# Performance work log

Hardware: AMD Instinct MI355X
Metric: run time of the kernel (lower is better)

The kernel has to match this reference:

```python
import jax, jax.numpy as jnp
import numpy as np


def conv1x1(x, w, b):
    # x: [B,C,H,W], w: [O,C], b: [O] -> [B,O,H,W]
    return jnp.einsum('bchw,oc->bohw', x, w) + b[None, :, None, None]


def setup_inputs() -> dict:
    key = jax.random.key(0)
    ks = jax.random.split(key, 8)
    B, C, H, W = 16, 256, 64, 64
    Cq = C // 8
    x = jax.random.normal(ks[0], (B, C, H, W), dtype=jnp.float32)
    wq = jax.random.normal(ks[1], (Cq, C), dtype=jnp.float32) * (2.0 / C) ** 0.5
    bq = jnp.zeros((Cq,), dtype=jnp.float32)
    wk = jax.random.normal(ks[2], (Cq, C), dtype=jnp.float32) * (2.0 / C) ** 0.5
    bk = jnp.zeros((Cq,), dtype=jnp.float32)
    wv = jax.random.normal(ks[3], (C, C), dtype=jnp.float32) * (2.0 / C) ** 0.5
    bv = jnp.zeros((C,), dtype=jnp.float32)
    gamma = jax.random.normal(ks[4], (1,), dtype=jnp.float32) * 0.1
    return {'x': x, 'wq': wq, 'bq': bq, 'wk': wk, 'bk': bk, 'wv': wv, 'bv': bv, 'gamma': gamma}


def reference(x, wq, bq, wk, bk, wv, bv, gamma):
    B, C, H, W = x.shape
    bH = B // 4
    bW = B // 4  # requires bH*bW == B, i.e. B == 16
    q = conv1x1(x, wq, bq)   # [B, C/8, H, W]
    k = conv1x1(x, wk, bk)   # [B, C/8, H, W]
    v = conv1x1(x, wv, bv)   # [B, C, H, W]
    # batch index b -> grid (h = b // bW, w = b % bW); token feature = flat map
    qg = q.reshape(bH, bW, -1)  # [bH, bW, Dq]
    kg = k.reshape(bH, bW, -1)
    vg = v.reshape(bH, bW, -1)  # [bH, bW, Dv]
    # column ('H') attention with -inf diagonal, row ('W') attention
    eH = jnp.einsum('hwd,gwd->hwg', qg, kg)  # [bH, bW, bH]
    eye = jnp.eye(bH, dtype=bool)[:, None, :]  # mask h == h'
    eH = jnp.where(eye, -jnp.inf, eH)
    eW = jnp.einsum('hwd,hgd->hwg', qg, kg)  # [bH, bW, bW]
    att = jax.nn.softmax(jnp.concatenate([eH, eW], axis=-1), axis=-1)
    aH, aW = att[..., :bH], att[..., bH:]
    oH = jnp.einsum('hwg,gwd->hwd', aH, vg)  # attend down the column
    oW = jnp.einsum('hwg,hgd->hwd', aW, vg)  # attend along the row
    out = (oH + oW).reshape(B, C, H, W)
    return gamma[0] * out + x
```

## Files before the change

kernel.cpp:

```cpp
#include <hip/hip_runtime.h>

#define HW_  4096
#define DV   1048576

using bf16x8 = __attribute__((ext_vector_type(8))) __bf16;
using f32x4  = __attribute__((ext_vector_type(4))) float;

static __device__ __forceinline__ unsigned short f2bf(float f) {
    union { float f; unsigned u; } v; v.f = f;
    unsigned r = v.u + 0x7FFFu + ((v.u >> 16) & 1u);
    return (unsigned short)(r >> 16);
}
static __device__ __forceinline__ float bf2f(unsigned short h) {
    union { unsigned u; float f; } v; v.u = ((unsigned)h) << 16;
    return v.f;
}

__global__ __launch_bounds__(256) void k_pack(const float* wq, const float* wk, const float* wv,
                                              unsigned short* WhF, unsigned short* WlF, unsigned short* WvF) {
    int idx = blockIdx.x * 256 + threadIdx.x;
    if (idx < 16384) {
        int i = idx;
        int mt = i >> 12, cg = (i >> 7) & 31, ml = (i >> 3) & 15, cl = i & 7;
        int m = mt * 16 + ml, c = cg * 8 + cl;
        float f = (m < 32) ? wq[m * 256 + c] : wk[(m - 32) * 256 + c];
        unsigned short hi = f2bf(f);
        WhF[i] = hi;
        WlF[i] = f2bf(f - bf2f(hi));
    } else {
        int i = idx - 16384;
        int mt = i >> 12, kt = (i >> 7) & 31, lr = (i >> 3) & 15, j = i & 7;
        int m = mt * 16 + lr, c = kt * 8 + j;
        WvF[i] = f2bf(wv[m * 256 + c]);
    }
}

__global__ __launch_bounds__(1024, 4) void k_qks(const unsigned short* __restrict__ WhF,
                                                 const unsigned short* __restrict__ WlF,
                                                 const float* __restrict__ x,
                                                 const float* __restrict__ bq, const float* __restrict__ bk,
                                                 float* __restrict__ Sp) {
    __shared__ __align__(16) __bf16 SB[2][16][2][1024];
    int n0 = blockIdx.x * 16;
    int t = threadIdx.x;
    int lane = t & 63, wid = t >> 6;
    int lr = lane & 15, kg = lane >> 4;
    int sn = t & 15, sk = t >> 4;
    int saddr = ((sk >> 3) * 16 + sn) * 8 + (sk & 7);

    f32x4 acc[4];
    #pragma unroll
    for (int mf = 0; mf < 4; mf++) acc[mf] = (f32x4){0.f, 0.f, 0.f, 0.f};

    float xv[16];
    const float* xs0 = x + (size_t)sk * HW_ + n0 + sn;
    #pragma unroll
    for (int bp = 0; bp < 16; bp++) xv[bp] = xs0[(size_t)bp * DV];
    #pragma unroll
    for (int bp = 0; bp < 16; bp++) {
        float v = xv[bp]; __bf16 h = (__bf16)v;
        SB[0][bp][0][saddr] = h;
        SB[0][bp][1][saddr] = (__bf16)(v - (float)h);
    }
    __syncthreads();

    const unsigned short* Abh = WhF + lane * 8;
    const unsigned short* Abl = WlF + lane * 8;

    for (int c = 0; c < 4; c++) {
        int cur = c & 1;
        if (c < 3) {
            const float* xp = x + (size_t)((c + 1) * 64 + sk) * HW_ + n0 + sn;
            #pragma unroll
            for (int bp = 0; bp < 16; bp++) xv[bp] = xp[(size_t)bp * DV];
        }
        #pragma unroll
        for (int sub = 0; sub < 2; sub++) {
            int kcg = c * 2 + sub;
            bf16x8 bh = *(const bf16x8*)&SB[cur][wid][0][sub * 512 + lane * 8];
            bf16x8 bl = *(const bf16x8*)&SB[cur][wid][1][sub * 512 + lane * 8];
            #pragma unroll
            for (int mf = 0; mf < 4; mf++) {
                bf16x8 ah = *(const bf16x8*)(Abh + mf * 4096 + kcg * 512);
                bf16x8 al = *(const bf16x8*)(Abl + mf * 4096 + kcg * 512);
                acc[mf] = __builtin_amdgcn_mfma_f32_16x16x32_bf16(ah, bh, acc[mf], 0, 0, 0);
                acc[mf] = __builtin_amdgcn_mfma_f32_16x16x32_bf16(ah, bl, acc[mf], 0, 0, 0);
                acc[mf] = __builtin_amdgcn_mfma_f32_16x16x32_bf16(al, bh, acc[mf], 0, 0, 0);
            }
        }
        if (c < 3) {
            int nb = cur ^ 1;
            #pragma unroll
            for (int bp = 0; bp < 16; bp++) {
                float v = xv[bp]; __bf16 h = (__bf16)v;
                SB[nb][bp][0][saddr] = h;
                SB[nb][bp][1][saddr] = (__bf16)(v - (float)h);
            }
        }
        __syncthreads();
    }

    __bf16* F = &SB[0][0][0][0];
    int b = wid;
    #pragma unroll
    for (int mf = 0; mf < 4; mf++) {
        #pragma unroll
        for (int i = 0; i < 4; i++) {
            int row64 = mf * 16 + kg * 4 + i;
            float val = acc[mf][i] + ((row64 < 32) ? bq[row64] : bk[row64 - 32]);
            int qk = row64 >> 5;
            int r  = row64 & 31;
            int col = r * 16 + lr;
            __bf16 h = (__bf16)val;
            __bf16 l = (__bf16)(val - (float)h);
            int base = qk * 16384 + ((col >> 3) * 16 + b) * 8 + (col & 7);
            F[base] = h;
            F[base + 8192] = l;
        }
    }
    __syncthreads();

    if (wid == 0) {
        f32x4 S = (f32x4){0.f, 0.f, 0.f, 0.f};
        #pragma unroll
        for (int s = 0; s < 16; s++) {
            bf16x8 qh = *(const bf16x8*)&F[s * 512 + lane * 8];
            bf16x8 ql = *(const bf16x8*)&F[8192 + s * 512 + lane * 8];
            bf16x8 kh = *(const bf16x8*)&F[16384 + s * 512 + lane * 8];
            bf16x8 kl = *(const bf16x8*)&F[24576 + s * 512 + lane * 8];
            S = __builtin_amdgcn_mfma_f32_16x16x32_bf16(qh, kh, S, 0, 0, 0);
            S = __builtin_amdgcn_mfma_f32_16x16x32_bf16(qh, kl, S, 0, 0, 0);
            S = __builtin_amdgcn_mfma_f32_16x16x32_bf16(ql, kh, S, 0, 0, 0);
        }
        #pragma unroll
        for (int i = 0; i < 4; i++) {
            int bb = kg * 4 + i;
            int bp = lr;
            int h = bb >> 2, w = bb & 3;
            float val = S[i];
            if ((bp & 3) == w) Sp[(size_t)blockIdx.x * 128 + bb * 8 + (bp >> 2)] = val;
            if ((bp >> 2) == h) Sp[(size_t)blockIdx.x * 128 + bb * 8 + 4 + (bp & 3)] = val;
        }
    }
}

__global__ void k_softmax3(const float* __restrict__ Sp, const float* __restrict__ gamma,
                           float* __restrict__ Mm) {
    __shared__ float SS[128];
    int t = threadIdx.x;
    float s = 0.f;
    #pragma unroll 8
    for (int blk = 0; blk < 256; blk++) s += Sp[(size_t)blk * 128 + t];
    SS[t] = s;
    __syncthreads();
    if (t < 16) {
        int b = t, h = b >> 2, w = b & 3;
        float e[8];
        for (int j = 0; j < 8; j++) e[j] = SS[b * 8 + j];
        e[h] = -INFINITY;
        float mx = e[0];
        for (int j = 1; j < 8; j++) mx = fmaxf(mx, e[j]);
        float aa[8], sum = 0.f;
        for (int j = 0; j < 8; j++) { aa[j] = expf(e[j] - mx); sum += aa[j]; }
        float inv = 1.0f / sum;
        float g = gamma[0];
        float row[16];
        for (int c = 0; c < 16; c++) row[c] = 0.f;
        for (int gg = 0; gg < 4; gg++) if (gg != h) row[gg * 4 + w] += aa[gg] * inv;
        for (int gg = 0; gg < 4; gg++) row[h * 4 + gg] += aa[4 + gg] * inv;
        for (int c = 0; c < 16; c++) Mm[b * 16 + c] = row[c] * g;
        Mm[256 + b] = g;
    }
}

__global__ __launch_bounds__(1024, 4) void k_fused(const unsigned short* __restrict__ WvF,
                                                   const float* __restrict__ x,
                                                   const float* __restrict__ bv,
                                                   const float* __restrict__ Mm,
                                                   float* __restrict__ out) {
    __shared__ __align__(16) __bf16 XB[2][16][1024];
    int n0 = blockIdx.x * 16;
    int t = threadIdx.x;
    int lane = t & 63, wid = t >> 6;
    int lr = lane & 15, kg = lane >> 4;
    int sn = t & 15, sk = t >> 4;
    int saddr = ((sk >> 3) * 16 + sn) * 8 + (sk & 7);

    f32x4 u[16];
    #pragma unroll
    for (int b = 0; b < 16; b++) u[b] = (f32x4){0.f, 0.f, 0.f, 0.f};

    float xv[16];
    const float* xs0 = x + (size_t)sk * HW_ + n0 + sn;
    #pragma unroll
    for (int bp = 0; bp < 16; bp++) xv[bp] = xs0[(size_t)bp * DV];
    #pragma unroll
    for (int bp = 0; bp < 16; bp++) XB[0][bp][saddr] = (__bf16)xv[bp];
    __syncthreads();

    const unsigned short* Ab = WvF + (size_t)wid * 4096 + lane * 8;

    for (int c = 0; c < 4; c++) {
        int cur = c & 1;
        if (c < 3) {
            const float* xp = x + (size_t)((c + 1) * 64 + sk) * HW_ + n0 + sn;
            #pragma unroll
            for (int bp = 0; bp < 16; bp++) xv[bp] = xp[(size_t)bp * DV];
        }
        #pragma unroll
        for (int sub = 0; sub < 2; sub++) {
            bf16x8 a = *(const bf16x8*)(Ab + (c * 2 + sub) * 512);
            #pragma unroll
            for (int b = 0; b < 16; b++) {
                bf16x8 bb = *(const bf16x8*)&XB[cur][b][sub * 512 + lane * 8];
                u[b] = __builtin_amdgcn_mfma_f32_16x16x32_bf16(a, bb, u[b], 0, 0, 0);
            }
        }
        if (c < 3) {
            int nb = cur ^ 1;
            #pragma unroll
            for (int bp = 0; bp < 16; bp++) XB[nb][bp][saddr] = (__bf16)xv[bp];
        }
        __syncthreads();
    }

    #pragma unroll
    for (int b = 0; b < 16; b++) {
        int h = b >> 2, w = b & 3;
        f32x4 m = (f32x4){0.f, 0.f, 0.f, 0.f};
        #pragma unroll
        for (int g = 0; g < 4; g++) {
            if (g != h) m += Mm[b * 16 + g * 4 + w] * u[g * 4 + w];
            m += Mm[b * 16 + h * 4 + g] * u[h * 4 + g];
        }
        float rs = Mm[256 + b];
        #pragma unroll
        for (int i = 0; i < 4; i++) {
            int mrow = wid * 16 + kg * 4 + i;
            size_t idx = (size_t)b * DV + (size_t)mrow * HW_ + n0 + lr;
            out[idx] = m[i] + rs * bv[mrow] + x[idx];
        }
    }
}

extern "C" void kernel_launch(void* const* d_in, const int* in_sizes, int n_in,
                              void* d_out, int out_size, void* d_ws, size_t ws_size,
                              hipStream_t stream) {
    (void)in_sizes; (void)n_in; (void)out_size; (void)ws_size;
    const float* x     = (const float*)d_in[0];
    const float* wq    = (const float*)d_in[1];
    const float* bq    = (const float*)d_in[2];
    const float* wk    = (const float*)d_in[3];
    const float* bk    = (const float*)d_in[4];
    const float* wv    = (const float*)d_in[5];
    const float* bv    = (const float*)d_in[6];
    const float* gamma = (const float*)d_in[7];

    char* ws = (char*)d_ws;
    unsigned short* WhF = (unsigned short*)(ws + 0);
    unsigned short* WlF = (unsigned short*)(ws + 32768);
    unsigned short* WvF = (unsigned short*)(ws + 65536);
    float*          Sp  = (float*)(ws + 196608);
    float*          Mm  = (float*)(ws + 327680);
    float*          vo  = (float*)d_out;

    k_pack     <<<320, 256, 0, stream>>>(wq, wk, wv, WhF, WlF, WvF);
    k_qks      <<<256, 1024, 0, stream>>>(WhF, WlF, x, bq, bk, Sp);
    k_softmax3 <<<1, 128, 0, stream>>>(Sp, gamma, Mm);
    k_fused    <<<256, 1024, 0, stream>>>(WvF, x, bv, Mm, vo);
}
```

Before: 103.2 us.

## Retile fused value kernel to 64x64 output tiles with vectorized loads and LDS-staged stores

The fused V-projection kernel now gives each block a 64-channel by 64-pixel tile across all 16 batches, instead of all 256 channels by 16 pixels. It iterates over 8 k-chunks with a swizzled LDS layout and float4 global loads of x. Output is staged through LDS so the residual add and final store run as coalesced float4 accesses. The Q/K score kernel also switches to float4 loads with a permuted LDS layout, and the partial-score buffer is transposed so the softmax reduction reads contiguous float4. The cost is a 128KB LDS footprint per block, which may reduce occupancy, plus extra LDS round trips in the epilogue.

```diff
diff --git a/kernel.cpp b/kernel.cpp
--- a/kernel.cpp
+++ b/kernel.cpp
@@ -40,27 +40,34 @@
                                                  const float* __restrict__ x,
                                                  const float* __restrict__ bq, const float* __restrict__ bk,
                                                  float* __restrict__ Sp) {
-    __shared__ __align__(16) __bf16 SB[2][16][2][1024];
+    __shared__ __align__(16) __bf16 SBf[2 * 16 * 2 * 1024];
     int n0 = blockIdx.x * 16;
     int t = threadIdx.x;
     int lane = t & 63, wid = t >> 6;
     int lr = lane & 15, kg = lane >> 4;
-    int sn = t & 15, sk = t >> 4;
-    int saddr = ((sk >> 3) * 16 + sn) * 8 + (sk & 7);
+    int n4 = t & 3, sk = (t >> 2) & 63, bpg = t >> 8;
+    int siglr = ((lr & 3) << 2) | (lr >> 2);
 
     f32x4 acc[4];
     #pragma unroll
     for (int mf = 0; mf < 4; mf++) acc[mf] = (f32x4){0.f, 0.f, 0.f, 0.f};
 
-    float xv[16];
-    const float* xs0 = x + (size_t)sk * HW_ + n0 + sn;
-    #pragma unroll
-    for (int bp = 0; bp < 16; bp++) xv[bp] = xs0[(size_t)bp * DV];
-    #pragma unroll
-    for (int bp = 0; bp < 16; bp++) {
-        float v = xv[bp]; __bf16 h = (__bf16)v;
-        SB[0][bp][0][saddr] = h;
-        SB[0][bp][1][saddr] = (__bf16)(v - (float)h);
+    f32x4 xv[4];
+    #pragma unroll
+    for (int bpi = 0; bpi < 4; bpi++)
+        xv[bpi] = *(const f32x4*)(x + (size_t)(bpg * 4 + bpi) * DV + (size_t)sk * HW_ + n0 + n4 * 4);
+    #pragma unroll
+    for (int bpi = 0; bpi < 4; bpi++) {
+        int bp = bpg * 4 + bpi;
+        __bf16* basep = SBf + ((0 * 16 + bp) * 2) * 1024 + (sk >> 5) * 512 + (((sk & 31) >> 3) * 16) * 8 + (sk & 7);
+        #pragma unroll
+        for (int e = 0; e < 4; e++) {
+            float v = xv[bpi][e];
+            __bf16 h = (__bf16)v;
+            int off = ((e << 2) | n4) * 8;
+            basep[off] = h;
+            basep[off + 1024] = (__bf16)(v - (float)h);
+        }
     }
     __syncthreads();
 
@@ -70,15 +77,16 @@
     for (int c = 0; c < 4; c++) {
         int cur = c & 1;
         if (c < 3) {
-            const float* xp = x + (size_t)((c + 1) * 64 + sk) * HW_ + n0 + sn;
-            #pragma unroll
-            for (int bp = 0; bp < 16; bp++) xv[bp] = xp[(size_t)bp * DV];
+            #pragma unroll
+            for (int bpi = 0; bpi < 4; bpi++)
+                xv[bpi] = *(const f32x4*)(x + (size_t)(bpg * 4 + bpi) * DV + (size_t)((c + 1) * 64 + sk) * HW_ + n0 + n4 * 4);
         }
         #pragma unroll
         for (int sub = 0; sub < 2; sub++) {
             int kcg = c * 2 + sub;
-            bf16x8 bh = *(const bf16x8*)&SB[cur][wid][0][sub * 512 + lane * 8];
-            bf16x8 bl = *(const bf16x8*)&SB[cur][wid][1][sub * 512 + lane * 8];
+            const __bf16* bptr = SBf + ((cur * 16 + wid) * 2) * 1024 + sub * 512 + (kg * 16 + siglr) * 8;
+            bf16x8 bh = *(const bf16x8*)bptr;
+            bf16x8 bl = *(const bf16x8*)(bptr + 1024);
             #pragma unroll
             for (int mf = 0; mf < 4; mf++) {
                 bf16x8 ah = *(const bf16x8*)(Abh + mf * 4096 + kcg * 512);
@@ -91,16 +99,23 @@
         if (c < 3) {
             int nb = cur ^ 1;
             #pragma unroll
-            for (int bp = 0; bp < 16; bp++) {
-                float v = xv[bp]; __bf16 h = (__bf16)v;
-                SB[nb][bp][0][saddr] = h;
-                SB[nb][bp][1][saddr] = (__bf16)(v - (float)h);
+            for (int bpi = 0; bpi < 4; bpi++) {
+                int bp = bpg * 4 + bpi;
+                __bf16* basep = SBf + ((nb * 16 + bp) * 2) * 1024 + (sk >> 5) * 512 + (((sk & 31) >> 3) * 16) * 8 + (sk & 7);
+                #pragma unroll
+                for (int e = 0; e < 4; e++) {
+                    float v = xv[bpi][e];
+                    __bf16 h = (__bf16)v;
+                    int off = ((e << 2) | n4) * 8;
+                    basep[off] = h;
+                    basep[off + 1024] = (__bf16)(v - (float)h);
+                }
             }
         }
         __syncthreads();
     }
 
-    __bf16* F = &SB[0][0][0][0];
+    __bf16* F = SBf;
     int b = wid;
     #pragma unroll
     for (int mf = 0; mf < 4; mf++) {
@@ -138,8 +153,8 @@
             int bp = lr;
             int h = bb >> 2, w = bb & 3;
             float val = S[i];
-            if ((bp & 3) == w) Sp[(size_t)blockIdx.x * 128 + bb * 8 + (bp >> 2)] = val;
-            if ((bp >> 2) == h) Sp[(size_t)blockIdx.x * 128 + bb * 8 + 4 + (bp & 3)] = val;
+            if ((bp & 3) == w)  Sp[(size_t)(bb * 8 + (bp >> 2)) * 256 + blockIdx.x] = val;
+            if ((bp >> 2) == h) Sp[(size_t)(bb * 8 + 4 + (bp & 3)) * 256 + blockIdx.x] = val;
         }
     }
 }
@@ -148,10 +163,11 @@
                            float* __restrict__ Mm) {
     __shared__ float SS[128];
     int t = threadIdx.x;
-    float s = 0.f;
+    const f32x4* s4 = (const f32x4*)(Sp + (size_t)t * 256);
+    f32x4 a = (f32x4){0.f, 0.f, 0.f, 0.f};
     #pragma unroll 8
-    for (int blk = 0; blk < 256; blk++) s += Sp[(size_t)blk * 128 + t];
-    SS[t] = s;
+    for (int i = 0; i < 64; i++) a += s4[i];
+    SS[t] = a[0] + a[1] + a[2] + a[3];
     __syncthreads();
     if (t < 16) {
         int b = t, h = b >> 2, w = b & 3;
@@ -178,68 +194,101 @@
                                                    const float* __restrict__ bv,
                                                    const float* __restrict__ Mm,
                                                    float* __restrict__ out) {
-    __shared__ __align__(16) __bf16 XB[2][16][1024];
-    int n0 = blockIdx.x * 16;
+    __shared__ __align__(16) char RAW[131072];
+    __bf16* XBf = (__bf16*)RAW;
+    int bid = blockIdx.x;
+    int xg = bid & 7, r = bid >> 3;
+    int nblk = xg * 8 + (r >> 2), mblk = r & 3;
+    int n0 = nblk * 64, m0 = mblk * 64;
     int t = threadIdx.x;
     int lane = t & 63, wid = t >> 6;
+    int wm = wid & 3, wn = wid >> 2;
     int lr = lane & 15, kg = lane >> 4;
-    int sn = t & 15, sk = t >> 4;
-    int saddr = ((sk >> 3) * 16 + sn) * 8 + (sk & 7);
+    int n4 = t & 15, sk = (t >> 4) & 31, bpg = t >> 9;
+    int sigr = (((lr & 3) << 2) | (lr >> 2)) ^ (wn << 1);
 
     f32x4 u[16];
     #pragma unroll
     for (int b = 0; b < 16; b++) u[b] = (f32x4){0.f, 0.f, 0.f, 0.f};
 
-    float xv[16];
-    const float* xs0 = x + (size_t)sk * HW_ + n0 + sn;
-    #pragma unroll
-    for (int bp = 0; bp < 16; bp++) xv[bp] = xs0[(size_t)bp * DV];
-    #pragma unroll
-    for (int bp = 0; bp < 16; bp++) XB[0][bp][saddr] = (__bf16)xv[bp];
+    f32x4 xv[8];
+    #pragma unroll
+    for (int bpi = 0; bpi < 8; bpi++)
+        xv[bpi] = *(const f32x4*)(x + (size_t)(bpg * 8 + bpi) * DV + (size_t)sk * HW_ + n0 + n4 * 4);
+    #pragma unroll
+    for (int bpi = 0; bpi < 8; bpi++) {
+        int bp = bpg * 8 + bpi;
+        __bf16* basep = XBf + ((0 * 16 + bp) * 4 + (n4 >> 2)) * 512 + ((sk >> 3) * 16) * 8 + (sk & 7);
+        #pragma unroll
+        for (int e = 0; e < 4; e++) {
+            int s = ((e << 2) | (n4 & 3)) ^ ((n4 >> 2) << 1);
+            basep[s * 8] = (__bf16)xv[bpi][e];
+        }
+    }
     __syncthreads();
 
-    const unsigned short* Ab = WvF + (size_t)wid * 4096 + lane * 8;
-
-    for (int c = 0; c < 4; c++) {
+    for (int c = 0; c < 8; c++) {
         int cur = c & 1;
-        if (c < 3) {
-            const float* xp = x + (size_t)((c + 1) * 64 + sk) * HW_ + n0 + sn;
-            #pragma unroll
-            for (int bp = 0; bp < 16; bp++) xv[bp] = xp[(size_t)bp * DV];
-        }
-        #pragma unroll
-        for (int sub = 0; sub < 2; sub++) {
-            bf16x8 a = *(const bf16x8*)(Ab + (c * 2 + sub) * 512);
-            #pragma unroll
-            for (int b = 0; b < 16; b++) {
-                bf16x8 bb = *(const bf16x8*)&XB[cur][b][sub * 512 + lane * 8];
-                u[b] = __builtin_amdgcn_mfma_f32_16x16x32_bf16(a, bb, u[b], 0, 0, 0);
-            }
-        }
-        if (c < 3) {
+        if (c < 7) {
+            #pragma unroll
+            for (int bpi = 0; bpi < 8; bpi++)
+                xv[bpi] = *(const f32x4*)(x + (size_t)(bpg * 8 + bpi) * DV + (size_t)((c + 1) * 32 + sk) * HW_ + n0 + n4 * 4);
+        }
+        bf16x8 a = *(const bf16x8*)(WvF + (size_t)(mblk * 4 + wm) * 4096 + c * 512 + lane * 8);
+        const __bf16* bbase = XBf + ((cur * 16) * 4 + wn) * 512 + (kg * 16 + sigr) * 8;
+        #pragma unroll
+        for (int bp = 0; bp < 16; bp++) {
+            bf16x8 bb = *(const bf16x8*)(bbase + bp * 2048);
+            u[bp] = __builtin_amdgcn_mfma_f32_16x16x32_bf16(a, bb, u[bp], 0, 0, 0);
+        }
+        if (c < 7) {
             int nb = cur ^ 1;
             #pragma unroll
-            for (int bp = 0; bp < 16; bp++) XB[nb][bp][saddr] = (__bf16)xv[bp];
+            for (int bpi = 0; bpi < 8; bpi++) {
+                int bp = bpg * 8 + bpi;
+                __bf16* basep = XBf + ((nb * 16 + bp) * 4 + (n4 >> 2)) * 512 + ((sk >> 3) * 16) * 8 + (sk & 7);
+                #pragma unroll
+                for (int e = 0; e < 4; e++) {
+                    int s = ((e << 2) | (n4 & 3)) ^ ((n4 >> 2) << 1);
+                    basep[s * 8] = (__bf16)xv[bpi][e];
+                }
+            }
         }
         __syncthreads();
     }
 
-    #pragma unroll
-    for (int b = 0; b < 16; b++) {
-        int h = b >> 2, w = b & 3;
-        f32x4 m = (f32x4){0.f, 0.f, 0.f, 0.f};
-        #pragma unroll
-        for (int g = 0; g < 4; g++) {
-            if (g != h) m += Mm[b * 16 + g * 4 + w] * u[g * 4 + w];
-            m += Mm[b * 16 + h * 4 + g] * u[h * 4 + g];
-        }
-        float rs = Mm[256 + b];
-        #pragma unroll
-        for (int i = 0; i < 4; i++) {
-            int mrow = wid * 16 + kg * 4 + i;
-            size_t idx = (size_t)b * DV + (size_t)mrow * HW_ + n0 + lr;
-            out[idx] = m[i] + rs * bv[mrow] + x[idx];
-        }
+    int mrow0 = m0 + wm * 16 + kg * 4;
+    f32x4 bv4 = (f32x4){bv[mrow0], bv[mrow0 + 1], bv[mrow0 + 2], bv[mrow0 + 3]};
+    float* LD = (float*)RAW;
+    int b2 = t >> 8, mr = (t >> 2) & 63, nq = t & 3;
+    for (int bg = 0; bg < 4; bg++) {
+        #pragma unroll
+        for (int bi = 0; bi < 4; bi++) {
+            int b = bg * 4 + bi, h = b >> 2, w = b & 3;
+            f32x4 mo = (f32x4){0.f, 0.f, 0.f, 0.f};
+            #pragma unroll
+            for (int g = 0; g < 4; g++) {
+                if (g != h) mo += Mm[b * 16 + g * 4 + w] * u[g * 4 + w];
+                mo += Mm[b * 16 + h * 4 + g] * u[h * 4 + g];
+            }
+            mo += Mm[256 + b] * bv4;
+            float* ld = LD + ((size_t)bi * 64 + wm * 16 + kg * 4) * 68 + wn * 16 + lr;
+            #pragma unroll
+            for (int i = 0; i < 4; i++) ld[i * 68] = mo[i];
+        }
+        __syncthreads();
+        {
+            int b = bg * 4 + b2;
+            const float* lrow = LD + ((size_t)b2 * 64 + mr) * 68 + nq * 16;
+            size_t gbase = (size_t)b * DV + (size_t)(m0 + mr) * HW_ + n0 + nq * 16;
+            #pragma unroll
+            for (int q = 0; q < 4; q++) {
+                f32x4 o  = *(const f32x4*)(lrow + q * 4);
+                f32x4 rr = *(const f32x4*)(x + gbase + q * 4);
+                *(f32x4*)(out + gbase + q * 4) = o + rr;
+            }
+        }
+        __syncthreads();
     }
 }
 
```

New measurement: 98.44 us. 1.05x faster.
